# Performance work log

Measured on AMD Instinct MI355X. Metric: run time of the kernel, lower is better.

## Reference

```python
import jax, jax.numpy as jnp
import numpy as np

# node types: 0=claim, 1=evidence, 2=user
N = [100_000, 150_000, 50_000]
E = 200_000                      # edges per edge type
ET = [(1, 0), (2, 0), (0, 1), (0, 2)]  # (src_type, dst_type)
HID, HEADS = 128, 4
DH = HID // HEADS
NUM_CLASSES = 3
NT = 3


def setup_inputs() -> dict:
    key = jax.random.key(0)
    ks = iter(jax.random.split(key, 64))
    inp = {}
    for t, n in enumerate(N):
        inp[f"x{t}"] = jax.random.normal(next(ks), (n, HID), jnp.float32)
    for e, (st, dt) in enumerate(ET):
        src = jax.random.randint(next(ks), (E,), 0, N[st], jnp.int32)
        dst = jax.random.randint(next(ks), (E,), 0, N[dt], jnp.int32)
        inp[f"ei{e}"] = jnp.stack([src, dst])
    def w(k, shape, fan_in):
        return jax.random.normal(k, shape, jnp.float32) / np.float32(np.sqrt(fan_in))
    for L in ("c1", "c2"):
        for nm in ("kw", "qw", "vw", "aw"):
            inp[f"{L}_{nm}"] = w(next(ks), (NT, HID, HID), HID)
        for nm in ("kb", "qb", "vb", "ab"):
            inp[f"{L}_{nm}"] = jnp.zeros((NT, HID), jnp.float32)
        inp[f"{L}_arel"] = w(next(ks), (len(ET), HEADS, DH, DH), DH)
        inp[f"{L}_mrel"] = w(next(ks), (len(ET), HEADS, DH, DH), DH)
        inp[f"{L}_prel"] = jnp.ones((len(ET), HEADS), jnp.float32)
        inp[f"{L}_skip"] = jnp.ones((NT,), jnp.float32)
    inp["lin_w"] = w(next(ks), (HID, NUM_CLASSES), HID)
    inp["lin_b"] = jnp.zeros((NUM_CLASSES,), jnp.float32)
    return inp


def _seg_softmax(a, seg, n):
    m = jax.ops.segment_max(a, seg, num_segments=n)
    ex = jnp.exp(a - m[seg])
    s = jax.ops.segment_sum(ex, seg, num_segments=n)
    return ex / (s[seg] + 1e-16)


def _hgt_conv(xs, eis, kw, kb, qw, qb, vw, vb, aw, ab, arel, mrel, prel, skip):
    # per-node-type K/Q/V projections -> [N_t, H, DH]
    k = [(xs[t] @ kw[t] + kb[t]).reshape(-1, HEADS, DH) for t in range(NT)]
    q = [(xs[t] @ qw[t] + qb[t]).reshape(-1, HEADS, DH) for t in range(NT)]
    v = [(xs[t] @ vw[t] + vb[t]).reshape(-1, HEADS, DH) for t in range(NT)]
    buckets = [[] for _ in range(NT)]  # per dst type: (alpha [E,H], dst [E], msg [E,H,DH])
    inv_sqrt_d = np.float32(1.0 / np.sqrt(DH))
    for e, (st, dt) in enumerate(ET):
        src, dst = eis[e][0], eis[e][1]
        ke = jnp.einsum('nhd,hde->nhe', k[st], arel[e])[src]
        ve = jnp.einsum('nhd,hde->nhe', v[st], mrel[e])[src]
        alpha = jnp.einsum('ehd,ehd->eh', q[dt][dst], ke) * prel[e] * inv_sqrt_d
        buckets[dt].append((alpha, dst, ve))
    outs = []
    for t in range(NT):
        alpha = jnp.concatenate([b[0] for b in buckets[t]], axis=0)
        dst = jnp.concatenate([b[1] for b in buckets[t]], axis=0)
        msg = jnp.concatenate([b[2] for b in buckets[t]], axis=0)
        a = _seg_softmax(alpha, dst, N[t])  # softmax over all incoming edges per dst node
        agg = jax.ops.segment_sum(msg * a[:, :, None], dst, num_segments=N[t])
        agg = agg.reshape(N[t], HID)
        o = jax.nn.gelu(agg, approximate=False) @ aw[t] + ab[t]
        s = jax.nn.sigmoid(skip[t])
        outs.append(s * o + (1.0 - s) * xs[t])
    return outs


def reference(x0, x1, x2, ei0, ei1, ei2, ei3,
              c1_kw, c1_kb, c1_qw, c1_qb, c1_vw, c1_vb, c1_aw, c1_ab,
              c1_arel, c1_mrel, c1_prel, c1_skip,
              c2_kw, c2_kb, c2_qw, c2_qb, c2_vw, c2_vb, c2_aw, c2_ab,
              c2_arel, c2_mrel, c2_prel, c2_skip,
              lin_w, lin_b):
    xs = [x0, x1, x2]
    eis = [ei0, ei1, ei2, ei3]
    xs = _hgt_conv(xs, eis, c1_kw, c1_kb, c1_qw, c1_qb, c1_vw, c1_vb, c1_aw, c1_ab,
                   c1_arel, c1_mrel, c1_prel, c1_skip)
    xs = [jax.nn.relu(x) for x in xs]
    xs = _hgt_conv(xs, eis, c2_kw, c2_kb, c2_qw, c2_qb, c2_vw, c2_vb, c2_aw, c2_ab,
                   c2_arel, c2_mrel, c2_prel, c2_skip)
    xs = [jax.nn.relu(x) for x in xs]
    out = xs[0] @ lin_w + lin_b  # logits on 'claim' nodes
    return (out, xs[0], xs[1], xs[2])
```

## Files before the change

### kernel.cpp

```cpp
#include <hip/hip_runtime.h>
#include <hip/hip_bf16.h>
#include <math.h>


typedef __bf16 bf16;
typedef __bf16 bf16x8 __attribute__((ext_vector_type(8)));
typedef float  f32x4  __attribute__((ext_vector_type(4)));

#define NE 200000
#define N0T 100000
#define N1T 150000
#define N2T 50000
#define BPITCH 136
#define QGELEMS 38400000
#define KSCALE (0.17677669529663687f * 1.4426950408889634f)

__device__ inline float bflo(unsigned u) { return __uint_as_float(u << 16); }
__device__ inline float bfhi(unsigned u) { return __uint_as_float(u & 0xFFFF0000u); }
__device__ inline unsigned f2bfbits(float f) {
    unsigned x = __float_as_uint(f);
    return ((x + 0x7FFFu + ((x >> 16) & 1u)) >> 16) & 0xFFFFu;
}
__device__ inline unsigned pk2(float a, float b) {
    return f2bfbits(a) | (f2bfbits(b) << 16);
}
__device__ inline float gelu_exact(float x) {
    return 0.5f * x * (1.0f + erff(x * 0.70710678118654752f));
}
__device__ inline float ldx(const void* p, size_t i, int f) {
    return f ? ((const float*)p)[i] : (float)((const bf16*)p)[i];
}

__device__ inline int plausible(float v) {
    float a = fabsf(v);
    return (v == 0.f) || (a > 1e-8f && a < 1e8f);
}

__global__ void detect_k(const void* p, int* flag) {
    __shared__ int cF, cB;
    int tid = threadIdx.x;
    if (tid == 0) { cF = 0; cB = 0; }
    __syncthreads();
    float vf = ((const float*)p)[tid];
    float b0 = (float)((const bf16*)p)[2 * tid];
    float b1 = (float)((const bf16*)p)[2 * tid + 1];
    if (plausible(vf)) atomicAdd(&cF, 1);
    if (plausible(b0) && plausible(b1)) atomicAdd(&cB, 1);
    __syncthreads();
    if (tid == 0) *flag = (cF > cB) ? 1 : 0;
}

__global__ void conv_f32_k(const void* src, float* dst, int n, const int* flagp) {
    int f = *flagp;
    int i = blockIdx.x * 256 + threadIdx.x;
    if (i >= n) return;
    dst[i] = ldx(src, i, f);
}

__global__ void transpose128f(const void* W, bf16* __restrict__ WT, const int* fwp) {
    int fw = *fwp;
    int gid = blockIdx.x * 256 + threadIdx.x;
    if (gid >= 3 * 16384) return;
    int t = gid >> 14, r = (gid >> 7) & 127, c = gid & 127;
    WT[gid] = (bf16)ldx(W, (size_t)(t << 14) + c * 128 + r, fw);
}

__global__ void prep_kv(const void* kw, const void* vw, const void* arel,
                        const void* mrel, const void* prel,
                        bf16* __restrict__ WkvT, const int* fwp) {
    int fw = *fwp;
    int gid = blockIdx.x * 256 + threadIdx.x;
    if (gid >= 4 * 2 * 128 * 128) return;
    int i = gid & 127;
    int j = (gid >> 7) & 127;
    int kind = (gid >> 14) & 1;
    int e = gid >> 15;
    const int stab[4] = {1, 2, 0, 0};
    int st = stab[e];
    int h = j >> 5, jj = j & 31;
    size_t wbase = (size_t)st * 16384;
    size_t rbase = (size_t)(e * 4 + h) * 1024;
    const void* w   = kind ? vw : kw;
    const void* rel = kind ? mrel : arel;
    float acc = 0.f;
    for (int d = 0; d < 32; ++d)
        acc += ldx(w, wbase + (size_t)i * 128 + h * 32 + d, fw) *
               ldx(rel, rbase + (size_t)d * 32 + jj, fw);
    if (!kind)
        acc *= ldx(prel, e * 4 + h, fw) * KSCALE;
    WkvT[((size_t)(e * 2 + kind) * 128 + j) * 128 + i] = (bf16)acc;
}

__global__ void prep_kvbias(const void* kb, const void* vb, const void* arel,
                            const void* mrel, const void* prel,
                            float* __restrict__ Bf, const int* fwp) {
    int fw = *fwp;
    int gid = blockIdx.x * 256 + threadIdx.x;
    if (gid >= 4 * 2 * 128) return;
    int j = gid & 127;
    int kind = (gid >> 7) & 1;
    int e = gid >> 8;
    const int stab[4] = {1, 2, 0, 0};
    int st = stab[e];
    int h = j >> 5, jj = j & 31;
    const void* b   = kind ? vb : kb;
    const void* rel = kind ? mrel : arel;
    float acc = 0.f;
    for (int d = 0; d < 32; ++d)
        acc += ldx(b, (size_t)st * 128 + h * 32 + d, fw) *
               ldx(rel, (size_t)(e * 4 + h) * 1024 + (size_t)d * 32 + jj, fw);
    if (!kind)
        acc *= ldx(prel, e * 4 + h, fw) * KSCALE;
    Bf[gid] = acc;
}

__global__ void zero_i32(int* p, int n) {
    int i = blockIdx.x * 256 + threadIdx.x;
    if (i < n) p[i] = 0;
}

__global__ void hist_k(const int* __restrict__ e0, const int* __restrict__ e1,
                       const int* __restrict__ e2, const int* __restrict__ e3,
                       int* c0, int* c1, int* c2) {
    int gid = blockIdx.x * 256 + threadIdx.x;
    if (gid >= 4 * NE) return;
    int e = gid / NE, i = gid - e * NE;
    const int* ep = (e == 0) ? e0 : (e == 1) ? e1 : (e == 2) ? e2 : e3;
    int dst = ep[NE + i];
    int* c = (e < 2) ? c0 : (e == 2) ? c1 : c2;
    atomicAdd(&c[dst], 1);
}

__global__ __launch_bounds__(256) void scan1(const int* __restrict__ cnt, int n,
                                             int* __restrict__ excl, int* __restrict__ bsums) {
    __shared__ int s[256];
    int tid = threadIdx.x;
    int base = blockIdx.x * 2048 + tid * 8;
    int v[8]; int tsum = 0;
    for (int j = 0; j < 8; ++j) {
        int idx = base + j;
        int c = (idx < n) ? cnt[idx] : 0;
        v[j] = c; tsum += c;
    }
    s[tid] = tsum; __syncthreads();
    for (int off = 1; off < 256; off <<= 1) {
        int t = 0; if (tid >= off) t = s[tid - off];
        __syncthreads(); s[tid] += t; __syncthreads();
    }
    int run = s[tid] - tsum;
    for (int j = 0; j < 8; ++j) {
        int idx = base + j;
        if (idx < n) excl[idx] = run;
        run += v[j];
    }
    if (tid == 255) bsums[blockIdx.x] = s[255];
}

__global__ void scan2(int* __restrict__ bs, int nb) {
    __shared__ int s[256];
    int tid = threadIdx.x;
    int v = (tid < nb) ? bs[tid] : 0;
    s[tid] = v; __syncthreads();
    for (int off = 1; off < 256; off <<= 1) {
        int t = 0; if (tid >= off) t = s[tid - off];
        __syncthreads(); s[tid] += t; __syncthreads();
    }
    if (tid < nb) bs[tid] = s[tid] - v;
}

__global__ void scan3(int* __restrict__ excl, const int* __restrict__ bs,
                      int* __restrict__ cursor, int n, int total) {
    int idx = blockIdx.x * 256 + threadIdx.x;
    if (idx < n) {
        int v = excl[idx] + bs[idx >> 11];
        excl[idx] = v;
        cursor[idx] = v;
    }
    if (idx == 0) excl[n] = total;
}

__global__ void fill_k(const int* __restrict__ e0, const int* __restrict__ e1,
                       const int* __restrict__ e2, const int* __restrict__ e3,
                       int* c0, int* c1, int* c2,
                       unsigned* a0, unsigned* a1, unsigned* a2,
                       int lb0, int lb1, int lb2, int lb3) {
    int gid = blockIdx.x * 256 + threadIdx.x;
    if (gid >= 4 * NE) return;
    int e = gid / NE, i = gid - e * NE;
    const int* ep = (e == 0) ? e0 : (e == 1) ? e1 : (e == 2) ? e2 : e3;
    int src = ep[i], dst = ep[NE + i];
    int lb = (e == 0) ? lb0 : (e == 1) ? lb1 : (e == 2) ? lb2 : lb3;
    int* c; unsigned* a;
    if (e < 2)      { c = c0; a = a0; }
    else if (e == 2){ c = c1; a = a1; }
    else            { c = c2; a = a2; }
    int pos = atomicAdd(&c[dst], 1);
    a[pos] = (unsigned)(lb + src);
}

__global__ __launch_bounds__(512) void proj_fused(
    const void* __restrict__ A, long aOff, int nrows,
    const bf16* __restrict__ Wb, const float* __restrict__ Bb,
    bf16* __restrict__ Ob, int ng,
    int w0, int w1, int w2, int b0, int b1, int b2,
    int o0, int o1, int o2, int p0, int p1, int p2,
    const int* fxp)
{
    int fx = *fxp;
    __shared__ bf16 sB[3 * 128 * BPITCH];
    __shared__ float sBias[3 * 128];
    int tid = threadIdx.x;
    #pragma unroll
    for (int g = 0; g < 3; ++g) {
        if (g >= ng) break;
        const bf16* wt = Wb + ((g == 0) ? w0 : (g == 1) ? w1 : w2);
        for (int it = 0; it < 4; ++it) {
            int idx = it * 512 + tid;
            int r = idx >> 4, c8 = idx & 15;
            *(bf16x8*)(&sB[(g * 128 + r) * BPITCH + c8 * 8]) =
                *(const bf16x8*)(wt + r * 128 + c8 * 8);
        }
    }
    if (tid < 384) {
        int g = tid >> 7, col = tid & 127;
        int bg = (g == 0) ? b0 : (g == 1) ? b1 : b2;
        sBias[tid] = Bb[bg + col];
    }
    __syncthreads();

    int lane = tid & 63, wave = tid >> 6;
    int quad = lane >> 4, n16 = lane & 15;

    int ntiles = (nrows + 127) >> 7;
    long tile = blockIdx.x;
    if (tile >= ntiles) return;

    float4 rf[8];
    bf16x8 rb[4];
    bf16x8 afr[4];

    auto issue = [&](long t) {
        long ar = t * 128 + wave * 16 + n16;
        if (ar >= nrows) ar = nrows - 1;
        size_t base = (size_t)aOff + (size_t)ar * 128 + quad * 8;
        if (fx) {
            const float* ap = (const float*)A + base;
            #pragma unroll
            for (int k = 0; k < 4; ++k) {
                rf[2 * k]     = *(const float4*)(ap + k * 32);
                rf[2 * k + 1] = *(const float4*)(ap + k * 32 + 4);
            }
        } else {
            const bf16* ap = (const bf16*)A + base;
            #pragma unroll
            for (int k = 0; k < 4; ++k) rb[k] = *(const bf16x8*)(ap + k * 32);
        }
    };
    auto cvt = [&]() {
        if (fx) {
            #pragma unroll
            for (int k = 0; k < 4; ++k) {
                float4 u = rf[2 * k], v = rf[2 * k + 1];
                bf16x8 t;
                t[0] = (bf16)u.x; t[1] = (bf16)u.y; t[2] = (bf16)u.z; t[3] = (bf16)u.w;
                t[4] = (bf16)v.x; t[5] = (bf16)v.y; t[6] = (bf16)v.z; t[7] = (bf16)v.w;
                afr[k] = t;
            }
        } else {
            #pragma unroll
            for (int k = 0; k < 4; ++k) afr[k] = rb[k];
        }
    };

    issue(tile);
    cvt();
    for (;;) {
        long next = tile + gridDim.x;
        bool more = (next < ntiles);
        if (more) issue(next);
        long row = tile * 128 + wave * 16 + n16;
        bool wr = (row < nrows);
        #pragma unroll
        for (int g = 0; g < 3; ++g) {
            if (g >= ng) break;
            bf16* op = Ob + ((g == 0) ? o0 : (g == 1) ? o1 : o2);
            int pg = (g == 0) ? p0 : (g == 1) ? p1 : p2;
            #pragma unroll
            for (int c = 0; c < 8; ++c) {
                f32x4 acc = {0.f, 0.f, 0.f, 0.f};
                const bf16* bp = &sB[(g * 128 + c * 16 + n16) * BPITCH + quad * 8];
                #pragma unroll
                for (int k = 0; k < 4; ++k)
                    acc = __builtin_amdgcn_mfma_f32_16x16x32_bf16(
                        *(const bf16x8*)(bp + k * 32), afr[k], acc, 0, 0, 0);
                if (wr) {
                    int colb = c * 16 + quad * 4;
                    float4 b4 = *(const float4*)(&sBias[g * 128 + colb]);
                    uint2 u;
                    u.x = pk2(acc[0] + b4.x, acc[1] + b4.y);
                    u.y = pk2(acc[2] + b4.z, acc[3] + b4.w);
                    *(uint2*)(op + (size_t)row * pg + colb) = u;
                }
            }
        }
        if (!more) break;
        cvt();
        tile = next;
    }
}

__global__ __launch_bounds__(256) void gemm_out(
    const bf16* __restrict__ G, long gOff, int nrows,
    const bf16* __restrict__ WT, const float* __restrict__ bias,
    void* __restrict__ out, long outOff,
    const void* __restrict__ xres, long xrOff,
    const float* __restrict__ skipv, const int* fxp)
{
    int fx = *fxp;
    __shared__ bf16 sB[128 * BPITCH];
    __shared__ float sBias[128];
    int tid = threadIdx.x;
    #pragma unroll
    for (int it = 0; it < 8; ++it) {
        int idx = it * 256 + tid;
        int r = idx >> 4, c8 = idx & 15;
        *(bf16x8*)(&sB[r * BPITCH + c8 * 8]) = *(const bf16x8*)(WT + r * 128 + c8 * 8);
    }
    if (tid < 128) sBias[tid] = bias[tid];
    __syncthreads();

    int lane = tid & 63, wave = tid >> 6;
    int quad = lane >> 4, n16 = lane & 15;
    float sk = skipv[0];
    float s = 1.f / (1.f + __expf(-sk));
    float os = 1.f - s;

    int ntiles = (nrows + 63) >> 6;
    long tile = blockIdx.x;
    if (tile >= ntiles) return;

    bf16x8 afr[4], nraw[4];
    auto issue = [&](long t) {
        long ar = t * 64 + wave * 16 + n16;
        if (ar >= nrows) ar = nrows - 1;
        const bf16* ap = G + gOff + (size_t)ar * 128 + quad * 8;
        nraw[0] = *(const bf16x8*)ap;
        nraw[1] = *(const bf16x8*)(ap + 32);
        nraw[2] = *(const bf16x8*)(ap + 64);
        nraw[3] = *(const bf16x8*)(ap + 96);
    };
    issue(tile);
    afr[0] = nraw[0]; afr[1] = nraw[1]; afr[2] = nraw[2]; afr[3] = nraw[3];

    for (;;) {
        long row = tile * 64 + wave * 16 + n16;
        bool wr = (row < nrows);
        long rc = wr ? row : (nrows - 1);
        long next = tile + gridDim.x;
        bool more = (next < ntiles);
        if (more) issue(next);
        float xrv[8][4];
        #pragma unroll
        for (int c = 0; c < 8; ++c) {
            size_t xi = (size_t)xrOff + (size_t)rc * 128 + c * 16 + quad * 4;
            if (fx) {
                float4 u = *(const float4*)((const float*)xres + xi);
                xrv[c][0] = u.x; xrv[c][1] = u.y; xrv[c][2] = u.z; xrv[c][3] = u.w;
            } else {
                uint2 u = *(const uint2*)((const bf16*)xres + xi);
                xrv[c][0] = bflo(u.x); xrv[c][1] = bfhi(u.x);
                xrv[c][2] = bflo(u.y); xrv[c][3] = bfhi(u.y);
            }
        }
        #pragma unroll
        for (int c = 0; c < 8; ++c) {
            f32x4 acc = {0.f, 0.f, 0.f, 0.f};
            const bf16* bp = &sB[(c * 16 + n16) * BPITCH + quad * 8];
            #pragma unroll
            for (int k = 0; k < 4; ++k)
                acc = __builtin_amdgcn_mfma_f32_16x16x32_bf16(
                    *(const bf16x8*)(bp + k * 32), afr[k], acc, 0, 0, 0);
            if (wr) {
                int colb = c * 16 + quad * 4;
                float4 b4 = *(const float4*)(&sBias[colb]);
                float v0 = fmaxf(s * (acc[0] + b4.x) + os * xrv[c][0], 0.f);
                float v1 = fmaxf(s * (acc[1] + b4.y) + os * xrv[c][1], 0.f);
                float v2 = fmaxf(s * (acc[2] + b4.z) + os * xrv[c][2], 0.f);
                float v3 = fmaxf(s * (acc[3] + b4.w) + os * xrv[c][3], 0.f);
                size_t oi = (size_t)outOff + (size_t)row * 128 + colb;
                if (fx) {
                    float4 u = {v0, v1, v2, v3};
                    *(float4*)((float*)out + oi) = u;
                } else {
                    uint2 u; u.x = pk2(v0, v1); u.y = pk2(v2, v3);
                    *(uint2*)((bf16*)out + oi) = u;
                }
            }
        }
        if (!more) break;
        afr[0] = nraw[0]; afr[1] = nraw[1]; afr[2] = nraw[2]; afr[3] = nraw[3];
        tile = next;
    }
}

#define AGG_UPD(M, L, A0, A1, P, VU)                                    \
    {                                                                   \
        float nm = fmaxf(M, P);                                         \
        float sc = exp2f(M - nm);                                       \
        float pe = exp2f(P - nm);                                       \
        L = L * sc + pe;                                                \
        A0 = A0 * sc + pe * bflo(VU);                                   \
        A1 = A1 * sc + pe * bfhi(VU);                                   \
        M = nm;                                                         \
    }

#define AGG_MERGE(M, L, A0, A1, MS, LS, AS0, AS1)                       \
    {                                                                   \
        float nm = fmaxf(M, MS);                                        \
        float s0 = exp2f(M - nm);                                       \
        float s1 = exp2f(MS - nm);                                      \
        L = L * s0 + LS * s1;                                           \
        A0 = A0 * s0 + AS0 * s1;                                        \
        A1 = A1 * s0 + AS1 * s1;                                        \
        M = nm;                                                         \
    }

__global__ __launch_bounds__(256) void edge_agg(
    const int* __restrict__ rp, const unsigned* __restrict__ adj,
    const bf16* Q, const bf16* __restrict__ KEVE, bf16* G, int n) {
    int lane = threadIdx.x & 63;
    int node = blockIdx.x * 4 + (threadIdx.x >> 6);
    if (node >= n) return;
    unsigned qu = *(const unsigned*)(Q + (size_t)node * 128 + lane * 2);
    float q0 = bflo(qu), q1 = bfhi(qu);
    int beg = rp[node], end = rp[node + 1];

    float m0 = -3.4e38f, l0 = 0.f, x00 = 0.f, x01 = 0.f;
    float m1 = -3.4e38f, l1 = 0.f, x10 = 0.f, x11 = 0.f;
    float m2 = -3.4e38f, l2 = 0.f, x20 = 0.f, x21 = 0.f;
    float m3 = -3.4e38f, l3 = 0.f, x30 = 0.f, x31 = 0.f;

    int i = beg;
    for (; i + 4 <= end; i += 4) {
        unsigned r0 = adj[i], r1 = adj[i + 1], r2 = adj[i + 2], r3 = adj[i + 3];
        const bf16* k0 = KEVE + (size_t)r0 * 256;
        const bf16* k1 = KEVE + (size_t)r1 * 256;
        const bf16* k2 = KEVE + (size_t)r2 * 256;
        const bf16* k3 = KEVE + (size_t)r3 * 256;
        unsigned ku0 = *(const unsigned*)(k0 + lane * 2);
        unsigned ku1 = *(const unsigned*)(k1 + lane * 2);
        unsigned ku2 = *(const unsigned*)(k2 + lane * 2);
        unsigned ku3 = *(const unsigned*)(k3 + lane * 2);
        unsigned vu0 = *(const unsigned*)(k0 + 128 + lane * 2);
        unsigned vu1 = *(const unsigned*)(k1 + 128 + lane * 2);
        unsigned vu2 = *(const unsigned*)(k2 + 128 + lane * 2);
        unsigned vu3 = *(const unsigned*)(k3 + 128 + lane * 2);
        float p0 = q0 * bflo(ku0) + q1 * bfhi(ku0);
        float p1 = q0 * bflo(ku1) + q1 * bfhi(ku1);
        float p2 = q0 * bflo(ku2) + q1 * bfhi(ku2);
        float p3 = q0 * bflo(ku3) + q1 * bfhi(ku3);
        p0 += __shfl_xor(p0, 1); p1 += __shfl_xor(p1, 1);
        p2 += __shfl_xor(p2, 1); p3 += __shfl_xor(p3, 1);
        p0 += __shfl_xor(p0, 2); p1 += __shfl_xor(p1, 2);
        p2 += __shfl_xor(p2, 2); p3 += __shfl_xor(p3, 2);
        p0 += __shfl_xor(p0, 4); p1 += __shfl_xor(p1, 4);
        p2 += __shfl_xor(p2, 4); p3 += __shfl_xor(p3, 4);
        p0 += __shfl_xor(p0, 8); p1 += __shfl_xor(p1, 8);
        p2 += __shfl_xor(p2, 8); p3 += __shfl_xor(p3, 8);
        AGG_UPD(m0, l0, x00, x01, p0, vu0);
        AGG_UPD(m1, l1, x10, x11, p1, vu1);
        AGG_UPD(m2, l2, x20, x21, p2, vu2);
        AGG_UPD(m3, l3, x30, x31, p3, vu3);
    }
    for (; i < end; ++i) {
        unsigned r0 = adj[i];
        const bf16* k0 = KEVE + (size_t)r0 * 256;
        unsigned ku0 = *(const unsigned*)(k0 + lane * 2);
        unsigned vu0 = *(const unsigned*)(k0 + 128 + lane * 2);
        float p0 = q0 * bflo(ku0) + q1 * bfhi(ku0);
        p0 += __shfl_xor(p0, 1);
        p0 += __shfl_xor(p0, 2);
        p0 += __shfl_xor(p0, 4);
        p0 += __shfl_xor(p0, 8);
        AGG_UPD(m0, l0, x00, x01, p0, vu0);
    }
    AGG_MERGE(m0, l0, x00, x01, m1, l1, x10, x11);
    AGG_MERGE(m2, l2, x20, x21, m3, l3, x30, x31);
    AGG_MERGE(m0, l0, x00, x01, m2, l2, x20, x21);

    float inv = (end > beg) ? 1.f / l0 : 0.f;
    float g0 = gelu_exact(x00 * inv);
    float g1 = gelu_exact(x01 * inv);
    *(unsigned*)(G + (size_t)node * 128 + lane * 2) = f2bfbits(g0) | (f2bfbits(g1) << 16);
}

__global__ __launch_bounds__(256) void logits_k(
    const void* X, size_t xOff, const float* __restrict__ W,
    const float* __restrict__ B, void* out, int n, const int* fxp) {
    int fx = *fxp;
    int lane = threadIdx.x & 63;
    int node = blockIdx.x * 4 + (threadIdx.x >> 6);
    if (node >= n) return;
    size_t xb = xOff + (size_t)node * 128;
    int d0 = lane * 2;
    float x0 = ldx(X, xb + d0, fx), x1 = ldx(X, xb + d0 + 1, fx);
    float p0 = x0 * W[d0 * 3 + 0] + x1 * W[d0 * 3 + 3];
    float p1 = x0 * W[d0 * 3 + 1] + x1 * W[d0 * 3 + 4];
    float p2 = x0 * W[d0 * 3 + 2] + x1 * W[d0 * 3 + 5];
    for (int off = 1; off < 64; off <<= 1) {
        p0 += __shfl_xor(p0, off);
        p1 += __shfl_xor(p1, off);
        p2 += __shfl_xor(p2, off);
    }
    if (lane == 0) {
        p0 += B[0]; p1 += B[1]; p2 += B[2];
        if (p0 != p0) p0 = 12345.f; else if (fabsf(p0) > 1e30f) p0 = 54321.f;
        if (p1 != p1) p1 = 12345.f; else if (fabsf(p1) > 1e30f) p1 = 54321.f;
        if (p2 != p2) p2 = 12345.f; else if (fabsf(p2) > 1e30f) p2 = 54321.f;
        size_t ob = (size_t)node * 3;
        if (fx) {
            ((float*)out)[ob] = p0; ((float*)out)[ob + 1] = p1; ((float*)out)[ob + 2] = p2;
        } else {
            ((bf16*)out)[ob] = (bf16)p0; ((bf16*)out)[ob + 1] = (bf16)p1;
            ((bf16*)out)[ob + 2] = (bf16)p2;
        }
    }
}


extern "C" void kernel_launch(void* const* d_in, const int* in_sizes, int n_in,
                              void* d_out, int out_size, void* d_ws, size_t ws_size,
                              hipStream_t stream) {
    (void)n_in; (void)out_size;

    const void* x_in[3] = {d_in[0], d_in[1], d_in[2]};
    const int* ei[4] = {(const int*)d_in[3], (const int*)d_in[4],
                        (const int*)d_in[5], (const int*)d_in[6]};

    size_t KROWS = 400000;
    {
        size_t need = 0;
        auto acc = [&](size_t b) { need += (b + 255) & ~(size_t)255; };
        acc((300000ull * 128 + KROWS * 256) * 2);
        acc(2ull * 11 * 16384 * 2);
        acc(2ull * 3 * 16384 * 2);
        acc(2ull * 1408 * 4);
        acc(2ull * 384 * 4);
        acc(2ull * 3 * 4);
        acc(384ull * 4);
        acc(3ull * 4);
        acc(2ull * 4);
        acc(300000ull * 4);
        acc(300003ull * 4);
        acc(300000ull * 4);
        acc(800000ull * 4);
        acc(3ull * 256 * 4);
        if (need > ws_size) KROWS = 200000;
    }
    const int big = (KROWS == 400000);
    int lb[4];
    if (big) { lb[0] = 0; lb[1] = 150000; lb[2] = 200000; lb[3] = 300000; }
    else     { lb[0] = 0; lb[1] = 150000; lb[2] = 0;      lb[3] = 100000; }

    char* p = (char*)d_ws;
    auto alloc = [&](size_t b) { char* r = p; p += (b + 255) & ~(size_t)255; return r; };
    bf16*  QG    = (bf16*)alloc((300000ull * 128 + KROWS * 256) * 2);
    bf16*  KEVE  = QG + QGELEMS;
    bf16*  wpool = (bf16*)alloc(2ull * 11 * 16384 * 2);
    bf16*  WaT   = (bf16*)alloc(2ull * 3 * 16384 * 2);
    float* bpool = (float*)alloc(2ull * 1408 * 4);
    float* abC   = (float*)alloc(2ull * 384 * 4);
    float* skipC = (float*)alloc(2ull * 3 * 4);
    float* linwC = (float*)alloc(384ull * 4);
    float* linbC = (float*)alloc(3ull * 4);
    int*   flags = (int*)alloc(2ull * 4);
    int* counts  = (int*)alloc(300000ull * 4);
    int* rowptr  = (int*)alloc(300003ull * 4);
    int* cursor  = (int*)alloc(300000ull * 4);
    unsigned* adj = (unsigned*)alloc(800000ull * 4);
    int* bsum    = (int*)alloc(3ull * 256 * 4);

    int* fxp = flags;
    int* fwp = flags + 1;

    const int Ns[3]    = {N0T, N1T, N2T};
    const int baseN[3] = {0, 100000, 250000};
    const int tot[3]   = {400000, 200000, 200000};
    int* cn[3] = {counts, counts + 100000, counts + 250000};
    int* rp[3] = {rowptr, rowptr + 100001, rowptr + 250002};
    int* cu[3] = {cursor, cursor + 100000, cursor + 250000};
    unsigned* aj[3] = {adj, adj + 400000, adj + 600000};
    const long dxsOff[3] = {300000, 13100000, 32300000};

    detect_k<<<1, 256, 0, stream>>>(d_in[0], fxp);
    detect_k<<<1, 256, 0, stream>>>(d_in[7], fwp);

    for (int L = 0; L < 2; ++L) {
        int b = 7 + 12 * L;
        bool sig = (in_sizes[b + 1] == 384);
        int ikw, iqw, ivw, iaw, ikb, iqb, ivb, iab;
        if (sig) { ikw = b; ikb = b + 1; iqw = b + 2; iqb = b + 3;
                   ivw = b + 4; ivb = b + 5; iaw = b + 6; iab = b + 7; }
        else     { ikw = b; iqw = b + 1; ivw = b + 2; iaw = b + 3;
                   ikb = b + 4; iqb = b + 5; ivb = b + 6; iab = b + 7; }
        transpose128f<<<192, 256, 0, stream>>>(d_in[iqw], wpool + (size_t)L * 11 * 16384, fwp);
        transpose128f<<<192, 256, 0, stream>>>(d_in[iaw], WaT + (size_t)L * 49152, fwp);
        prep_kv<<<512, 256, 0, stream>>>(d_in[ikw], d_in[ivw], d_in[b + 8], d_in[b + 9],
                                         d_in[b + 10], wpool + ((size_t)L * 11 + 3) * 16384, fwp);
        prep_kvbias<<<4, 256, 0, stream>>>(d_in[ikb], d_in[ivb], d_in[b + 8], d_in[b + 9],
                                           d_in[b + 10], bpool + L * 1408 + 384, fwp);
        conv_f32_k<<<2, 256, 0, stream>>>(d_in[iqb], bpool + L * 1408, 384, fwp);
        conv_f32_k<<<2, 256, 0, stream>>>(d_in[iab], abC + L * 384, 384, fwp);
        conv_f32_k<<<1, 256, 0, stream>>>(d_in[b + 11], skipC + L * 3, 3, fwp);
    }
    conv_f32_k<<<2, 256, 0, stream>>>(d_in[31], linwC, 384, fwp);
    conv_f32_k<<<1, 256, 0, stream>>>(d_in[32], linbC, 3, fwp);

    zero_i32<<<1172, 256, 0, stream>>>(counts, 300000);
    hist_k<<<3125, 256, 0, stream>>>(ei[0], ei[1], ei[2], ei[3], cn[0], cn[1], cn[2]);
    for (int t = 0; t < 3; ++t) {
        int nb = (Ns[t] + 2047) / 2048;
        scan1<<<nb, 256, 0, stream>>>(cn[t], Ns[t], rp[t], bsum + t * 256);
        scan2<<<1, 256, 0, stream>>>(bsum + t * 256, nb);
        scan3<<<(Ns[t] + 255) / 256, 256, 0, stream>>>(rp[t], bsum + t * 256, cu[t], Ns[t], tot[t]);
    }
    fill_k<<<3125, 256, 0, stream>>>(ei[0], ei[1], ei[2], ei[3],
                                     cu[0], cu[1], cu[2], aj[0], aj[1], aj[2],
                                     lb[0], lb[1], lb[2], lb[3]);

    for (int L = 0; L < 2; ++L) {
        const void* xp[3]; long xo[3];
        for (int t = 0; t < 3; ++t) {
            xp[t] = L ? (const void*)d_out : x_in[t];
            xo[t] = L ? dxsOff[t] : 0;
        }

        auto WQi  = [&](int t) { return (L * 11 + t) * 16384; };
        auto WKVi = [&](int e, int k) { return (L * 11 + 3 + e * 2 + k) * 16384; };
        auto BQi  = [&](int t) { return L * 1408 + t * 128; };
        auto BKVi = [&](int e, int k) { return L * 1408 + 384 + (e * 2 + k) * 128; };
        auto OQ   = [&](int t) { return baseN[t] * 128; };
        auto OKe  = [&](int e) { return QGELEMS + lb[e] * 256; };

        auto proj = [&](int st, int ng,
                        int w0, int w1, int w2, int bb0, int bb1, int bb2,
                        int oo0, int oo1, int oo2, int pp0, int pp1, int pp2) {
            int nt = (Ns[st] + 127) / 128;
            int grid = nt < 512 ? nt : 512;
            proj_fused<<<grid, 512, 0, stream>>>(xp[st], xo[st], Ns[st],
                wpool, bpool, QG, ng, w0, w1, w2, bb0, bb1, bb2,
                oo0, oo1, oo2, pp0, pp1, pp2, fxp);
        };
        auto agg = [&](int t) {
            edge_agg<<<(Ns[t] + 3) / 4, 256, 0, stream>>>(
                rp[t], aj[t], QG + (size_t)baseN[t] * 128, KEVE,
                QG + (size_t)baseN[t] * 128, Ns[t]);
        };
        auto outp = [&](int t) {
            int nt = (Ns[t] + 63) / 64;
            int grid = nt < 512 ? nt : 512;
            gemm_out<<<grid, 256, 0, stream>>>(
                QG, (long)baseN[t] * 128, Ns[t],
                WaT + ((size_t)L * 3 + t) * 16384, abC + L * 384 + t * 128,
                d_out, dxsOff[t], xp[t], xo[t], skipC + L * 3 + t, fxp);
        };

        if (big) {
            proj(1, 3, WQi(1), WKVi(0, 0), WKVi(0, 1), BQi(1), BKVi(0, 0), BKVi(0, 1),
                 OQ(1), OKe(0), OKe(0) + 128, 128, 256, 256);
            proj(2, 3, WQi(2), WKVi(1, 0), WKVi(1, 1), BQi(2), BKVi(1, 0), BKVi(1, 1),
                 OQ(2), OKe(1), OKe(1) + 128, 128, 256, 256);
            proj(0, 3, WQi(0), WKVi(2, 0), WKVi(2, 1), BQi(0), BKVi(2, 0), BKVi(2, 1),
                 OQ(0), OKe(2), OKe(2) + 128, 128, 256, 256);
            proj(0, 2, WKVi(3, 0), WKVi(3, 1), WKVi(3, 1), BKVi(3, 0), BKVi(3, 1), BKVi(3, 1),
                 OKe(3), OKe(3) + 128, OKe(3) + 128, 256, 256, 256);
            agg(0); agg(1); agg(2);
        } else {
            proj(0, 1, WQi(0), WQi(0), WQi(0), BQi(0), BQi(0), BQi(0),
                 OQ(0), OQ(0), OQ(0), 128, 128, 128);
            proj(1, 3, WQi(1), WKVi(0, 0), WKVi(0, 1), BQi(1), BKVi(0, 0), BKVi(0, 1),
                 OQ(1), OKe(0), OKe(0) + 128, 128, 256, 256);
            proj(2, 3, WQi(2), WKVi(1, 0), WKVi(1, 1), BQi(2), BKVi(1, 0), BKVi(1, 1),
                 OQ(2), OKe(1), OKe(1) + 128, 128, 256, 256);
            agg(0);
            proj(0, 2, WKVi(2, 0), WKVi(2, 1), WKVi(2, 1), BKVi(2, 0), BKVi(2, 1), BKVi(2, 1),
                 OKe(2), OKe(2) + 128, OKe(2) + 128, 256, 256, 256);
            proj(0, 2, WKVi(3, 0), WKVi(3, 1), WKVi(3, 1), BKVi(3, 0), BKVi(3, 1), BKVi(3, 1),
                 OKe(3), OKe(3) + 128, OKe(3) + 128, 256, 256, 256);
            agg(1); agg(2);
        }
        outp(0); outp(1); outp(2);
    }

    logits_k<<<25000, 256, 0, stream>>>(d_out, dxsOff[0], linwC, linbC, d_out, N0T, fxp);
}
```

Before: 1.278 ms.

## Merge edge aggregation launches, use half-wave per node, double-buffer projection loads

The edge aggregation kernel now handles two destination nodes per wave, one per 32-lane half, with wider 8-byte loads per lane. A single launch covers all node types through a combined rowptr and adjacency buffer, replacing the per-type launches. The projection GEMM now keeps two tiles of A-row prefetches in flight, and its grid is capped at 256 blocks instead of 512. This aims to raise memory-level parallelism and cut launch overhead, at the cost of more registers and reliance on a concatenated graph layout.

```diff
diff --git a/kernel.cpp b/kernel.cpp
--- a/kernel.cpp
+++ b/kernel.cpp
@@ -232,14 +232,15 @@
     int quad = lane >> 4, n16 = lane & 15;
 
     int ntiles = (nrows + 127) >> 7;
-    long tile = blockIdx.x;
-    if (tile >= ntiles) return;
-
-    float4 rf[8];
-    bf16x8 rb[4];
+    long tA = blockIdx.x;
+    if (tA >= ntiles) return;
+    long G1 = gridDim.x, G2 = 2 * G1;
+
+    float4 rfA[8], rfB[8];
+    bf16x8 rbA[4], rbB[4];
     bf16x8 afr[4];
 
-    auto issue = [&](long t) {
+    auto issueA = [&](long t) {
         long ar = t * 128 + wave * 16 + n16;
         if (ar >= nrows) ar = nrows - 1;
         size_t base = (size_t)aOff + (size_t)ar * 128 + quad * 8;
@@ -247,20 +248,37 @@
             const float* ap = (const float*)A + base;
             #pragma unroll
             for (int k = 0; k < 4; ++k) {
-                rf[2 * k]     = *(const float4*)(ap + k * 32);
-                rf[2 * k + 1] = *(const float4*)(ap + k * 32 + 4);
+                rfA[2 * k]     = *(const float4*)(ap + k * 32);
+                rfA[2 * k + 1] = *(const float4*)(ap + k * 32 + 4);
             }
         } else {
             const bf16* ap = (const bf16*)A + base;
             #pragma unroll
-            for (int k = 0; k < 4; ++k) rb[k] = *(const bf16x8*)(ap + k * 32);
+            for (int k = 0; k < 4; ++k) rbA[k] = *(const bf16x8*)(ap + k * 32);
         }
     };
-    auto cvt = [&]() {
+    auto issueB = [&](long t) {
+        long ar = t * 128 + wave * 16 + n16;
+        if (ar >= nrows) ar = nrows - 1;
+        size_t base = (size_t)aOff + (size_t)ar * 128 + quad * 8;
         if (fx) {
+            const float* ap = (const float*)A + base;
             #pragma unroll
             for (int k = 0; k < 4; ++k) {
-                float4 u = rf[2 * k], v = rf[2 * k + 1];
+                rfB[2 * k]     = *(const float4*)(ap + k * 32);
+                rfB[2 * k + 1] = *(const float4*)(ap + k * 32 + 4);
+            }
+        } else {
+            const bf16* ap = (const bf16*)A + base;
+            #pragma unroll
+            for (int k = 0; k < 4; ++k) rbB[k] = *(const bf16x8*)(ap + k * 32);
+        }
+    };
+    auto cvtA = [&]() {
+        if (fx) {
+            #pragma unroll
+            for (int k = 0; k < 4; ++k) {
+                float4 u = rfA[2 * k], v = rfA[2 * k + 1];
                 bf16x8 t;
                 t[0] = (bf16)u.x; t[1] = (bf16)u.y; t[2] = (bf16)u.z; t[3] = (bf16)u.w;
                 t[4] = (bf16)v.x; t[5] = (bf16)v.y; t[6] = (bf16)v.z; t[7] = (bf16)v.w;
@@ -268,17 +286,26 @@
             }
         } else {
             #pragma unroll
-            for (int k = 0; k < 4; ++k) afr[k] = rb[k];
+            for (int k = 0; k < 4; ++k) afr[k] = rbA[k];
         }
     };
-
-    issue(tile);
-    cvt();
-    for (;;) {
-        long next = tile + gridDim.x;
-        bool more = (next < ntiles);
-        if (more) issue(next);
-        long row = tile * 128 + wave * 16 + n16;
+    auto cvtB = [&]() {
+        if (fx) {
+            #pragma unroll
+            for (int k = 0; k < 4; ++k) {
+                float4 u = rfB[2 * k], v = rfB[2 * k + 1];
+                bf16x8 t;
+                t[0] = (bf16)u.x; t[1] = (bf16)u.y; t[2] = (bf16)u.z; t[3] = (bf16)u.w;
+                t[4] = (bf16)v.x; t[5] = (bf16)v.y; t[6] = (bf16)v.z; t[7] = (bf16)v.w;
+                afr[k] = t;
+            }
+        } else {
+            #pragma unroll
+            for (int k = 0; k < 4; ++k) afr[k] = rbB[k];
+        }
+    };
+    auto compute = [&](long t) {
+        long row = t * 128 + wave * 16 + n16;
         bool wr = (row < nrows);
         #pragma unroll
         for (int g = 0; g < 3; ++g) {
@@ -303,9 +330,23 @@
                 }
             }
         }
-        if (!more) break;
-        cvt();
-        tile = next;
+    };
+
+    issueA(tA);
+    long tB = tA + G1;
+    bool hasB = tB < ntiles;
+    if (hasB) issueB(tB);
+    for (;;) {
+        cvtA();
+        if (tA + G2 < ntiles) issueA(tA + G2);
+        compute(tA);
+        if (!hasB) break;
+        cvtB();
+        if (tB + G2 < ntiles) issueB(tB + G2);
+        compute(tB);
+        tA += G2; tB += G2;
+        if (tA >= ntiles) break;
+        hasB = tB < ntiles;
     }
 }
 
@@ -403,42 +444,57 @@
     }
 }
 
-#define AGG_UPD(M, L, A0, A1, P, VU)                                    \
+#define UPD4(M, L, A0, A1, A2, A3, P, VU)                               \
     {                                                                   \
         float nm = fmaxf(M, P);                                         \
         float sc = exp2f(M - nm);                                       \
         float pe = exp2f(P - nm);                                       \
         L = L * sc + pe;                                                \
-        A0 = A0 * sc + pe * bflo(VU);                                   \
-        A1 = A1 * sc + pe * bfhi(VU);                                   \
+        A0 = A0 * sc + pe * bflo(VU.x);                                 \
+        A1 = A1 * sc + pe * bfhi(VU.x);                                 \
+        A2 = A2 * sc + pe * bflo(VU.y);                                 \
+        A3 = A3 * sc + pe * bfhi(VU.y);                                 \
         M = nm;                                                         \
     }
 
-#define AGG_MERGE(M, L, A0, A1, MS, LS, AS0, AS1)                       \
+#define MRG4(M, L, A0, A1, A2, A3, MS, LS, B0, B1, B2, B3)              \
     {                                                                   \
         float nm = fmaxf(M, MS);                                        \
         float s0 = exp2f(M - nm);                                       \
         float s1 = exp2f(MS - nm);                                      \
         L = L * s0 + LS * s1;                                           \
-        A0 = A0 * s0 + AS0 * s1;                                        \
-        A1 = A1 * s0 + AS1 * s1;                                        \
+        A0 = A0 * s0 + B0 * s1;                                         \
+        A1 = A1 * s0 + B1 * s1;                                         \
+        A2 = A2 * s0 + B2 * s1;                                         \
+        A3 = A3 * s0 + B3 * s1;                                         \
         M = nm;                                                         \
     }
 
-__global__ __launch_bounds__(256) void edge_agg(
-    const int* __restrict__ rp, const unsigned* __restrict__ adj,
-    const bf16* Q, const bf16* __restrict__ KEVE, bf16* G, int n) {
+__global__ __launch_bounds__(256) void edge_agg2(
+    const int* __restrict__ rowptr, const unsigned* __restrict__ adjb,
+    bf16* __restrict__ QG, const bf16* __restrict__ KEVE,
+    int g0, int nNodes) {
     int lane = threadIdx.x & 63;
-    int node = blockIdx.x * 4 + (threadIdx.x >> 6);
-    if (node >= n) return;
-    unsigned qu = *(const unsigned*)(Q + (size_t)node * 128 + lane * 2);
-    float q0 = bflo(qu), q1 = bfhi(qu);
-    int beg = rp[node], end = rp[node + 1];
-
-    float m0 = -3.4e38f, l0 = 0.f, x00 = 0.f, x01 = 0.f;
-    float m1 = -3.4e38f, l1 = 0.f, x10 = 0.f, x11 = 0.f;
-    float m2 = -3.4e38f, l2 = 0.f, x20 = 0.f, x21 = 0.f;
-    float m3 = -3.4e38f, l3 = 0.f, x30 = 0.f, x31 = 0.f;
+    int wave = threadIdx.x >> 6;
+    int sub = lane >> 5, l32 = lane & 31;
+    int gi = blockIdx.x * 8 + wave * 2 + sub;
+    if (gi >= nNodes) return;
+    int g = g0 + gi;
+    int t = (g >= 100000) + (g >= 250000);
+    const unsigned* adj = adjb + ((t == 0) ? 0u : (t == 1) ? 400000u : 600000u);
+    int amax = (t == 0) ? 400000 : 200000;
+    int rpi = g + t;
+    int beg = rowptr[rpi], end = rowptr[rpi + 1];
+    if (beg < 0) beg = 0;
+    if (end > amax) end = amax;
+
+    uint2 qu = *(const uint2*)(QG + (size_t)g * 128 + l32 * 4);
+    float q0 = bflo(qu.x), q1 = bfhi(qu.x), q2 = bflo(qu.y), q3 = bfhi(qu.y);
+
+    float m0 = -3.4e38f, l0 = 0.f, a00 = 0.f, a01 = 0.f, a02 = 0.f, a03 = 0.f;
+    float m1 = -3.4e38f, l1 = 0.f, a10 = 0.f, a11 = 0.f, a12 = 0.f, a13 = 0.f;
+    float m2 = -3.4e38f, l2 = 0.f, a20 = 0.f, a21 = 0.f, a22 = 0.f, a23 = 0.f;
+    float m3 = -3.4e38f, l3 = 0.f, a30 = 0.f, a31 = 0.f, a32 = 0.f, a33 = 0.f;
 
     int i = beg;
     for (; i + 4 <= end; i += 4) {
@@ -447,51 +503,51 @@
         const bf16* k1 = KEVE + (size_t)r1 * 256;
         const bf16* k2 = KEVE + (size_t)r2 * 256;
         const bf16* k3 = KEVE + (size_t)r3 * 256;
-        unsigned ku0 = *(const unsigned*)(k0 + lane * 2);
-        unsigned ku1 = *(const unsigned*)(k1 + lane * 2);
-        unsigned ku2 = *(const unsigned*)(k2 + lane * 2);
-        unsigned ku3 = *(const unsigned*)(k3 + lane * 2);
-        unsigned vu0 = *(const unsigned*)(k0 + 128 + lane * 2);
-        unsigned vu1 = *(const unsigned*)(k1 + 128 + lane * 2);
-        unsigned vu2 = *(const unsigned*)(k2 + 128 + lane * 2);
-        unsigned vu3 = *(const unsigned*)(k3 + 128 + lane * 2);
-        float p0 = q0 * bflo(ku0) + q1 * bfhi(ku0);
-        float p1 = q0 * bflo(ku1) + q1 * bfhi(ku1);
-        float p2 = q0 * bflo(ku2) + q1 * bfhi(ku2);
-        float p3 = q0 * bflo(ku3) + q1 * bfhi(ku3);
+        uint2 ku0 = *(const uint2*)(k0 + l32 * 4);
+        uint2 ku1 = *(const uint2*)(k1 + l32 * 4);
+        uint2 ku2 = *(const uint2*)(k2 + l32 * 4);
+        uint2 ku3 = *(const uint2*)(k3 + l32 * 4);
+        uint2 vu0 = *(const uint2*)(k0 + 128 + l32 * 4);
+        uint2 vu1 = *(const uint2*)(k1 + 128 + l32 * 4);
+        uint2 vu2 = *(const uint2*)(k2 + 128 + l32 * 4);
+        uint2 vu3 = *(const uint2*)(k3 + 128 + l32 * 4);
+        float p0 = q0 * bflo(ku0.x) + q1 * bfhi(ku0.x) + q2 * bflo(ku0.y) + q3 * bfhi(ku0.y);
+        float p1 = q0 * bflo(ku1.x) + q1 * bfhi(ku1.x) + q2 * bflo(ku1.y) + q3 * bfhi(ku1.y);
+        float p2 = q0 * bflo(ku2.x) + q1 * bfhi(ku2.x) + q2 * bflo(ku2.y) + q3 * bfhi(ku2.y);
+        float p3 = q0 * bflo(ku3.x) + q1 * bfhi(ku3.x) + q2 * bflo(ku3.y) + q3 * bfhi(ku3.y);
         p0 += __shfl_xor(p0, 1); p1 += __shfl_xor(p1, 1);
         p2 += __shfl_xor(p2, 1); p3 += __shfl_xor(p3, 1);
         p0 += __shfl_xor(p0, 2); p1 += __shfl_xor(p1, 2);
         p2 += __shfl_xor(p2, 2); p3 += __shfl_xor(p3, 2);
         p0 += __shfl_xor(p0, 4); p1 += __shfl_xor(p1, 4);
         p2 += __shfl_xor(p2, 4); p3 += __shfl_xor(p3, 4);
-        p0 += __shfl_xor(p0, 8); p1 += __shfl_xor(p1, 8);
-        p2 += __shfl_xor(p2, 8); p3 += __shfl_xor(p3, 8);
-        AGG_UPD(m0, l0, x00, x01, p0, vu0);
-        AGG_UPD(m1, l1, x10, x11, p1, vu1);
-        AGG_UPD(m2, l2, x20, x21, p2, vu2);
-        AGG_UPD(m3, l3, x30, x31, p3, vu3);
+        UPD4(m0, l0, a00, a01, a02, a03, p0, vu0);
+        UPD4(m1, l1, a10, a11, a12, a13, p1, vu1);
+        UPD4(m2, l2, a20, a21, a22, a23, p2, vu2);
+        UPD4(m3, l3, a30, a31, a32, a33, p3, vu3);
     }
     for (; i < end; ++i) {
         unsigned r0 = adj[i];
         const bf16* k0 = KEVE + (size_t)r0 * 256;
-        unsigned ku0 = *(const unsigned*)(k0 + lane * 2);
-        unsigned vu0 = *(const unsigned*)(k0 + 128 + lane * 2);
-        float p0 = q0 * bflo(ku0) + q1 * bfhi(ku0);
+        uint2 ku0 = *(const uint2*)(k0 + l32 * 4);
+        uint2 vu0 = *(const uint2*)(k0 + 128 + l32 * 4);
+        float p0 = q0 * bflo(ku0.x) + q1 * bfhi(ku0.x) + q2 * bflo(ku0.y) + q3 * bfhi(ku0.y);
         p0 += __shfl_xor(p0, 1);
         p0 += __shfl_xor(p0, 2);
         p0 += __shfl_xor(p0, 4);
-        p0 += __shfl_xor(p0, 8);
-        AGG_UPD(m0, l0, x00, x01, p0, vu0);
-    }
-    AGG_MERGE(m0, l0, x00, x01, m1, l1, x10, x11);
-    AGG_MERGE(m2, l2, x20, x21, m3, l3, x30, x31);
-    AGG_MERGE(m0, l0, x00, x01, m2, l2, x20, x21);
+        UPD4(m0, l0, a00, a01, a02, a03, p0, vu0);
+    }
+    MRG4(m0, l0, a00, a01, a02, a03, m1, l1, a10, a11, a12, a13);
+    MRG4(m2, l2, a20, a21, a22, a23, m3, l3, a30, a31, a32, a33);
+    MRG4(m0, l0, a00, a01, a02, a03, m2, l2, a20, a21, a22, a23);
 
     float inv = (end > beg) ? 1.f / l0 : 0.f;
-    float g0 = gelu_exact(x00 * inv);
-    float g1 = gelu_exact(x01 * inv);
-    *(unsigned*)(G + (size_t)node * 128 + lane * 2) = f2bfbits(g0) | (f2bfbits(g1) << 16);
+    float g0v = gelu_exact(a00 * inv);
+    float g1v = gelu_exact(a01 * inv);
+    float g2v = gelu_exact(a02 * inv);
+    float g3v = gelu_exact(a03 * inv);
+    uint2 u; u.x = pk2(g0v, g1v); u.y = pk2(g2v, g3v);
+    *(uint2*)(QG + (size_t)g * 128 + l32 * 4) = u;
 }
 
 __global__ __launch_bounds__(256) void logits_k(
@@ -646,15 +702,14 @@
                         int w0, int w1, int w2, int bb0, int bb1, int bb2,
                         int oo0, int oo1, int oo2, int pp0, int pp1, int pp2) {
             int nt = (Ns[st] + 127) / 128;
-            int grid = nt < 512 ? nt : 512;
+            int grid = nt < 256 ? nt : 256;
             proj_fused<<<grid, 512, 0, stream>>>(xp[st], xo[st], Ns[st],
                 wpool, bpool, QG, ng, w0, w1, w2, bb0, bb1, bb2,
                 oo0, oo1, oo2, pp0, pp1, pp2, fxp);
         };
-        auto agg = [&](int t) {
-            edge_agg<<<(Ns[t] + 3) / 4, 256, 0, stream>>>(
-                rp[t], aj[t], QG + (size_t)baseN[t] * 128, KEVE,
-                QG + (size_t)baseN[t] * 128, Ns[t]);
+        auto agg = [&](int g0, int nn) {
+            edge_agg2<<<(nn + 7) / 8, 256, 0, stream>>>(
+                rowptr, adj, QG, KEVE, g0, nn);
         };
         auto outp = [&](int t) {
             int nt = (Ns[t] + 63) / 64;
@@ -674,7 +729,7 @@
                  OQ(0), OKe(2), OKe(2) + 128, 128, 256, 256);
             proj(0, 2, WKVi(3, 0), WKVi(3, 1), WKVi(3, 1), BKVi(3, 0), BKVi(3, 1), BKVi(3, 1),
                  OKe(3), OKe(3) + 128, OKe(3) + 128, 256, 256, 256);
-            agg(0); agg(1); agg(2);
+            agg(0, 300000);
         } else {
             proj(0, 1, WQi(0), WQi(0), WQi(0), BQi(0), BQi(0), BQi(0),
                  OQ(0), OQ(0), OQ(0), 128, 128, 128);
@@ -682,12 +737,12 @@
                  OQ(1), OKe(0), OKe(0) + 128, 128, 256, 256);
             proj(2, 3, WQi(2), WKVi(1, 0), WKVi(1, 1), BQi(2), BKVi(1, 0), BKVi(1, 1),
                  OQ(2), OKe(1), OKe(1) + 128, 128, 256, 256);
-            agg(0);
+            agg(0, 100000);
             proj(0, 2, WKVi(2, 0), WKVi(2, 1), WKVi(2, 1), BKVi(2, 0), BKVi(2, 1), BKVi(2, 1),
                  OKe(2), OKe(2) + 128, OKe(2) + 128, 256, 256, 256);
             proj(0, 2, WKVi(3, 0), WKVi(3, 1), WKVi(3, 1), BKVi(3, 0), BKVi(3, 1), BKVi(3, 1),
                  OKe(3), OKe(3) + 128, OKe(3) + 128, 256, 256, 256);
-            agg(1); agg(2);
+            agg(100000, 200000);
         }
         outp(0); outp(1); outp(2);
     }
```

New measurement: 1.280 ms. About the same (+0.1%).
